# Optimization experiments

Hardware: AMD Instinct MI355X
Metric: run time of the kernel (lower is better)

Reference implementation:

```python
import jax, jax.numpy as jnp
import numpy as np

N = 100000      # nodes
F_IN = 512      # num_features
H = 256         # hidden
C = 64          # num_classes
E = 3200000     # edges
K = 10          # APPNP propagation steps
ALPHA = 0.1     # teleport probability


def setup_inputs() -> dict:
    key = jax.random.key(0)
    k_x, k_w0, k_w1, k_e = jax.random.split(key, 4)
    x = jax.random.normal(k_x, (N, F_IN), dtype=jnp.float32)
    w0 = jax.random.normal(k_w0, (F_IN, H), dtype=jnp.float32) / np.sqrt(F_IN).astype(np.float32)
    b0 = jnp.zeros((H,), dtype=jnp.float32)
    w1 = jax.random.normal(k_w1, (H, C), dtype=jnp.float32) / np.sqrt(H).astype(np.float32)
    b1 = jnpps = jnp.zeros((C,), dtype=jnp.float32)
    edge_index = jax.random.randint(k_e, (2, E), 0, N, dtype=jnp.int64)
    return {"x": x, "w0": w0, "b0": b0, "w1": w1, "b1": b1, "edge_index": edge_index}


def _appnp(h, edge_index):
    # Add self loops (PyG APPNP default: gcn_norm with self loops).
    loops = jnp.arange(N, dtype=edge_index.dtype)
    src = jnp.concatenate([edge_index[0], loops])
    dst = jnp.concatenate([edge_index[1], loops])
    # Symmetric GCN normalization: D^{-1/2} (A+I) D^{-1/2}
    deg = jax.ops.segment_sum(jnp.ones_like(src, dtype=h.dtype), dst, num_segments=N)
    dinv = jnp.where(deg > 0, jax.lax.rsqrt(deg), 0.0)
    norm = dinv[src] * dinv[dst]  # [E+N]

    def step(xc, _):
        msg = norm[:, None] * xc[src]                      # gather [E+N, C]
        agg = jax.ops.segment_sum(msg, dst, num_segments=N)  # scatter-add [N, C]
        return (1.0 - ALPHA) * agg + ALPHA * h, None

    out, _ = jax.lax.scan(step, h, None, length=K)
    return out


def reference(x, w0, b0, w1, b1, edge_index):
    # eval mode: dropout is identity
    h = jax.nn.relu(x @ w0 + b0)   # [N, H]
    h = h @ w1 + b1                # [N, C]
    z = _appnp(h, edge_index)      # [N, C]
    return jax.nn.log_softmax(z, axis=1)
```

## Files before the change

kernel.cpp:

```cpp
#include <hip/hip_runtime.h>
#include <hip/hip_bf16.h>

#define NN 100000
#define EE 3200000
#define FIN 512
#define HH 256
#define CC 64
#define KSTEPS 10
#define SB 391
#define NBUC 782
#define EPB 4096
#define NEB 782
#define NB_X2B 2048
#define NB_PREP 576

typedef __attribute__((ext_vector_type(8))) short bf16x8;
typedef __attribute__((ext_vector_type(8))) short s16x8;
typedef __attribute__((ext_vector_type(4))) float f32x4;
typedef unsigned short ushort_t;

__device__ __forceinline__ short f2bf(float f) {
    union { __hip_bfloat16 h; short s; } u;
    u.h = __float2bfloat16(f);
    return u.s;
}

__device__ __forceinline__ void glds16(const void* g, void* l) {
    __builtin_amdgcn_global_load_lds(
        (const __attribute__((address_space(1))) void*)g,
        (__attribute__((address_space(3))) void*)l, 16, 0, 0);
}


__device__ void dev_x2b(int bx, const float* __restrict__ x, ushort_t* __restrict__ xb) {
    const long NTOT = (long)NN * FIN;
    const long stride = (long)NB_X2B * 256 * 8;
    for (long i = ((long)bx * 256 + threadIdx.x) * 8; i < NTOT; i += stride) {
        float4 a = *(const float4*)(x + i);
        float4 b = *(const float4*)(x + i + 4);
        s16x8 o;
        o[0] = f2bf(a.x); o[1] = f2bf(a.y); o[2] = f2bf(a.z); o[3] = f2bf(a.w);
        o[4] = f2bf(b.x); o[5] = f2bf(b.y); o[6] = f2bf(b.z); o[7] = f2bf(b.w);
        *(s16x8*)(xb + i) = o;
    }
}

__device__ void dev_prep_w(int bx, const float* __restrict__ w0, const float* __restrict__ w1,
                           short* __restrict__ w0t, short* __restrict__ w1t) {
    int t = bx * 256 + threadIdx.x;
    if (t < FIN * HH) {
        int k = t >> 8, n = t & 255;
        w0t[n * FIN + k] = f2bf(w0[t]);
    } else if (t < FIN * HH + HH * CC) {
        int u = t - FIN * HH;
        int k = u >> 6, n = u & 63;
        w1t[n * HH + k] = f2bf(w1[u]);
    }
}

__device__ void dev_bincnt(int bx, const int* __restrict__ ei, int* __restrict__ bcnt,
                           int* __restrict__ hb) {
    int tid = threadIdx.x;
    int base = bx * EPB;
    for (int i = tid; i < NBUC; i += 256) hb[i] = 0;
    __syncthreads();
#pragma unroll 4
    for (int i = 0; i < EPB / 256; ++i) {
        int t = base + i * 256 + tid;
        if (t < EE) atomicAdd(&hb[(unsigned)ei[EE + t] >> 7], 1);
    }
    __syncthreads();
    for (int i = tid; i < NBUC; i += 256)
        if (hb[i]) atomicAdd(&bcnt[i], hb[i]);
}

__global__ __launch_bounds__(256) void fused1(const float* __restrict__ x,
                                              ushort_t* __restrict__ xb,
                                              const int* __restrict__ ei,
                                              int* __restrict__ bcnt,
                                              const float* __restrict__ w0,
                                              const float* __restrict__ w1,
                                              short* __restrict__ w0t,
                                              short* __restrict__ w1t) {
    __shared__ int hb[NBUC];
    int bx = blockIdx.x;
    if (bx < NB_X2B) dev_x2b(bx, x, xb);
    else if (bx < NB_X2B + NEB) dev_bincnt(bx - NB_X2B, ei, bcnt, hb);
    else dev_prep_w(bx - NB_X2B - NEB, w0, w1, w0t, w1t);
}


__global__ __launch_bounds__(1024) void bscan(const int* __restrict__ bcnt,
                                              int* __restrict__ eboff) {
    __shared__ int sh[1024];
    int t = threadIdx.x;
    int v = (t < NBUC) ? bcnt[t] : 0;
    sh[t] = v;
    __syncthreads();
    for (int off = 1; off < 1024; off <<= 1) {
        int add = (t >= off) ? sh[t - off] : 0;
        __syncthreads();
        sh[t] += add;
        __syncthreads();
    }
    if (t < NBUC) eboff[t] = sh[t] - v;
}

__device__ void dev_binfill(int bx, const int* __restrict__ ei, const int* __restrict__ eboff,
                            int* __restrict__ bfc, int* __restrict__ stg, int* pool) {
    int* hb = pool;
    int* lb = pool + NBUC;
    int tid = threadIdx.x;
    int base = bx * EPB;
    for (int i = tid; i < NBUC; i += 256) hb[i] = 0;
    __syncthreads();
#pragma unroll 4
    for (int i = 0; i < EPB / 256; ++i) {
        int t = base + i * 256 + tid;
        if (t < EE) atomicAdd(&hb[(unsigned)ei[EE + t] >> 7], 1);
    }
    __syncthreads();
    for (int i = tid; i < NBUC; i += 256) {
        int c = hb[i];
        lb[i] = eboff[i] + (c ? atomicAdd(&bfc[i], c) : 0);
        hb[i] = 0;
    }
    __syncthreads();
#pragma unroll 4
    for (int i = 0; i < EPB / 256; ++i) {
        int t = base + i * 256 + tid;
        if (t < EE) {
            int s = ei[t];
            int d = ei[EE + t];
            int b = (unsigned)d >> 7;
            int o = atomicAdd(&hb[b], 1);
            stg[lb[b] + o] = (s << 7) | (d & 127);
        }
    }
}

__device__ void dev_gemm1(int g1, const ushort_t* __restrict__ xb,
                          const short* __restrict__ w0t, const float* __restrict__ b0,
                          short* __restrict__ h0, char* sm) {
    short* AsP = (short*)sm;
    short* BsP = (short*)(sm + 32768);
    const int tid = threadIdx.x;
    const int lane = tid & 63;
    const int wid = tid >> 6;
    const int wm = wid >> 1, wn = wid & 1;
    const int bn0 = (g1 & 1) * 128;
    const long row0 = (long)(g1 >> 1) * 128;
    const int rl = lane >> 3;
    const int gko = (lane & 7) ^ rl;

    auto stage = [&](int kt, int buf) {
#pragma unroll
        for (int j = 0; j < 4; ++j) {
            int blk = wid * 4 + j;
            const ushort_t* g = xb + (row0 + blk * 8 + rl) * FIN + kt * 64 + gko * 8;
            glds16(g, &AsP[buf * 8192 + blk * 512]);
        }
#pragma unroll
        for (int j = 0; j < 4; ++j) {
            int blk = wid * 4 + j;
            const short* g = w0t + (size_t)(bn0 + blk * 8 + rl) * FIN + kt * 64 + gko * 8;
            glds16(g, &BsP[buf * 8192 + blk * 512]);
        }
    };

    f32x4 acc[4][4] = {};
    stage(0, 0);
    __syncthreads();
    for (int kt = 0; kt < FIN / 64; ++kt) {
        int cur = kt & 1;
        if (kt < FIN / 64 - 1) stage(kt + 1, cur ^ 1);
#pragma unroll
        for (int ks = 0; ks < 2; ++ks) {
            int ko = ks * 4 + (lane >> 4);
            int slot = ko ^ (lane & 7);
            bf16x8 af[4], bfr[4];
#pragma unroll
            for (int i = 0; i < 4; ++i) {
                int row = wm * 64 + i * 16 + (lane & 15);
                af[i] = *(const bf16x8*)(&AsP[cur * 8192 + (row * 8 + slot) * 8]);
            }
#pragma unroll
            for (int j = 0; j < 4; ++j) {
                int col = wn * 64 + j * 16 + (lane & 15);
                bfr[j] = *(const bf16x8*)(&BsP[cur * 8192 + (col * 8 + slot) * 8]);
            }
#pragma unroll
            for (int i = 0; i < 4; ++i)
#pragma unroll
                for (int j = 0; j < 4; ++j)
                    acc[i][j] = __builtin_amdgcn_mfma_f32_16x16x32_bf16(af[i], bfr[j], acc[i][j], 0, 0, 0);
        }
        __syncthreads();
    }
#pragma unroll
    for (int j = 0; j < 4; ++j) {
        int gcol = bn0 + wn * 64 + j * 16 + (lane & 15);
        float bias = b0[gcol];
#pragma unroll
        for (int i = 0; i < 4; ++i)
#pragma unroll
            for (int q = 0; q < 4; ++q) {
                long grow = row0 + wm * 64 + i * 16 + (lane >> 4) * 4 + q;
                float v = acc[i][j][q] + bias;
                if (v < 0.f) v = 0.f;
                h0[grow * HH + gcol] = f2bf(v);
            }
    }
}

__global__ __launch_bounds__(256) void fused3(const int* __restrict__ ei,
                                              const int* __restrict__ eboff,
                                              int* __restrict__ bfc,
                                              int* __restrict__ stg,
                                              const ushort_t* __restrict__ xb,
                                              const short* __restrict__ w0t,
                                              const float* __restrict__ b0,
                                              short* __restrict__ h0) {
    __shared__ __align__(16) char sm[65536];
    int bx = blockIdx.x, r = bx % 3, q = bx / 3;
    if (r == 2) dev_binfill(q, ei, eboff, bfc, stg, (int*)sm);
    else dev_gemm1(q * 2 + r, xb, w0t, b0, h0, sm);
}

__global__ __launch_bounds__(256) void bucket_finish(
    const int* __restrict__ stg, const int* __restrict__ eboff,
    const int* __restrict__ bcnt,
    int* __restrict__ cnt, float* __restrict__ dinv, float* __restrict__ wco,
    float* __restrict__ sdg, int* __restrict__ rp, int* __restrict__ eds,
    int* __restrict__ dbc) {
    __shared__ int nc8[128 * 8];
    __shared__ int nc[128];
    __shared__ int sc[128];
    __shared__ int lrp[128];
    __shared__ int h64[64];
    int b = blockIdx.x, tid = threadIdx.x;
    int nodes = min(128, NN - b * 128);
    for (int i = tid; i < 128 * 8; i += 256) nc8[i] = 0;
    if (tid < 64) h64[tid] = 0;
    __syncthreads();
    int s0 = eboff[b], n = bcnt[b];
    for (int i = tid; i < n; i += 256) {
        int e = stg[s0 + i];
        atomicAdd(&nc8[(e & 127) * 8 + ((e >> 7) >> 14)], 1);
    }
    __syncthreads();
    if (tid < 128) {
        int excl = 0;
#pragma unroll
        for (int r = 0; r < 8; ++r) {
            int c = nc8[tid * 8 + r];
            nc8[tid * 8 + r] = excl;
            excl += c;
        }
        nc[tid] = excl;
        sc[tid] = (tid < nodes) ? excl + 1 : 0;
    }
    __syncthreads();
    for (int off = 1; off < 128; off <<= 1) {
        int add = (tid < 128 && tid >= off) ? sc[tid - off] : 0;
        __syncthreads();
        if (tid < 128) sc[tid] += add;
        __syncthreads();
    }
    int base = eboff[b] + b * 128;
    if (tid < nodes) {
        int node = b * 128 + tid;
        int c = nc[tid];
        int excl = base + sc[tid] - (c + 1);
        lrp[tid] = excl;
        rp[node] = excl;
        cnt[node] = c;
        float fd = (float)(c + 1);
        dinv[node] = rsqrtf(fd);
        wco[node] = 0.9f / fd;
        sdg[node] = sqrtf(fd);
        atomicAdd(&h64[min(c, 63)], 1);
    }
    if (b == NBUC - 1 && tid == 0) rp[NN] = base + n + nodes;
    __syncthreads();
    if (tid < 64 && h64[tid]) atomicAdd(&dbc[tid], h64[tid]);
    for (int i = tid; i < n; i += 256) {
        int e = stg[s0 + i];
        int src = e >> 7, loc = e & 127;
        int o = atomicAdd(&nc8[loc * 8 + (src >> 14)], 1);
        eds[lrp[loc] + o] = src;
    }
    __syncthreads();
    if (tid < nodes) eds[lrp[tid] + nc[tid]] = b * 128 + tid;
}

__global__ void dscan(const int* __restrict__ dbc, int* __restrict__ dboff) {
    __shared__ int sh[64];
    int t = threadIdx.x;
    int v = dbc[t];
    sh[t] = v;
    __syncthreads();
    for (int off = 1; off < 64; off <<= 1) {
        int add = (t >= off) ? sh[t - off] : 0;
        __syncthreads();
        sh[t] += add;
        __syncthreads();
    }
    dboff[t] = sh[t] - v;
}

__global__ __launch_bounds__(256) void dperm(const int* __restrict__ cnt,
                                             const int* __restrict__ dboff,
                                             int* __restrict__ dfc,
                                             int* __restrict__ perm) {
    __shared__ int h[64];
    __shared__ int base[64];
    int tid = threadIdx.x;
    int i = blockIdx.x * 256 + tid;
    if (tid < 64) h[tid] = 0;
    __syncthreads();
    int bin = 0, r = 0;
    bool ok = i < NN;
    if (ok) {
        bin = min(cnt[i], 63);
        r = atomicAdd(&h[bin], 1);
    }
    __syncthreads();
    if (tid < 64) {
        int c = h[tid];
        base[tid] = dboff[tid] + (c ? atomicAdd(&dfc[tid], c) : 0);
    }
    __syncthreads();
    if (ok) perm[base[bin] + r] = i;
}

__global__ __launch_bounds__(256) void gemm2(const short* __restrict__ h0,
                                             const short* __restrict__ w1t,
                                             const float* __restrict__ b1,
                                             const float* __restrict__ dinv,
                                             ushort_t* __restrict__ hvb,
                                             ushort_t* __restrict__ v0) {
    __shared__ __align__(16) short As[2][128 * 64];
    __shared__ __align__(16) short Bs[2][64 * 64];
    const int tid = threadIdx.x;
    const int lane = tid & 63;
    const int wid = tid >> 6;
    const int wm = wid >> 1, wn = wid & 1;
    const long row0 = (long)blockIdx.x * 128;
    const int rl = lane >> 3;
    const int gko = (lane & 7) ^ rl;

    auto stage = [&](int kt, int buf) {
#pragma unroll
        for (int j = 0; j < 4; ++j) {
            int blk = wid * 4 + j;
            const short* g = h0 + (row0 + blk * 8 + rl) * HH + kt * 64 + gko * 8;
            glds16(g, &As[buf][blk * 512]);
        }
#pragma unroll
        for (int j = 0; j < 2; ++j) {
            int blk = wid * 2 + j;
            const short* g = w1t + (size_t)(blk * 8 + rl) * HH + kt * 64 + gko * 8;
            glds16(g, &Bs[buf][blk * 512]);
        }
    };

    f32x4 acc[4][2] = {};
    stage(0, 0);
    __syncthreads();
    for (int kt = 0; kt < HH / 64; ++kt) {
        int cur = kt & 1;
        if (kt < HH / 64 - 1) stage(kt + 1, cur ^ 1);
#pragma unroll
        for (int ks = 0; ks < 2; ++ks) {
            int ko = ks * 4 + (lane >> 4);
            int slot = ko ^ (lane & 7);
            bf16x8 af[4], bfr[2];
#pragma unroll
            for (int i = 0; i < 4; ++i) {
                int row = wm * 64 + i * 16 + (lane & 15);
                af[i] = *(const bf16x8*)(&As[cur][(row * 8 + slot) * 8]);
            }
#pragma unroll
            for (int j = 0; j < 2; ++j) {
                int col = wn * 32 + j * 16 + (lane & 15);
                bfr[j] = *(const bf16x8*)(&Bs[cur][(col * 8 + slot) * 8]);
            }
#pragma unroll
            for (int i = 0; i < 4; ++i)
#pragma unroll
                for (int j = 0; j < 2; ++j)
                    acc[i][j] = __builtin_amdgcn_mfma_f32_16x16x32_bf16(af[i], bfr[j], acc[i][j], 0, 0, 0);
        }
        __syncthreads();
    }
#pragma unroll
    for (int i = 0; i < 4; ++i)
#pragma unroll
        for (int j = 0; j < 2; ++j) {
            int col = wn * 32 + j * 16 + (lane & 15);
            float bias = b1[col];
#pragma unroll
            for (int q = 0; q < 4; ++q) {
                long grow = row0 + wm * 64 + i * 16 + (lane >> 4) * 4 + q;
                if (grow < NN) {
                    float hval = acc[i][j][q] + bias;
                    float dv = dinv[grow];
                    hvb[grow * CC + col] = (ushort_t)f2bf(0.1f * dv * hval);
                    v0[grow * CC + col] = (ushort_t)f2bf(dv * hval);
                }
            }
        }
}

__device__ __forceinline__ int2 grow2(const ushort_t* __restrict__ vin, int src, int l) {
    return *(const int2*)(vin + ((size_t)src << 6) + (l << 2));
}
__device__ __forceinline__ void acc2(float a[4], int2 r) {
    a[0] += __int_as_float(r.x << 16);
    a[1] += __int_as_float(r.x & 0xffff0000);
    a[2] += __int_as_float(r.y << 16);
    a[3] += __int_as_float(r.y & 0xffff0000);
}

template <int LAST>
__global__ __launch_bounds__(256) void prop(const ushort_t* __restrict__ vin,
                                            const ushort_t* __restrict__ hvb,
                                            const float* __restrict__ wco,
                                            const float* __restrict__ sdg,
                                            ushort_t* __restrict__ vout,
                                            float* __restrict__ zout,
                                            const int* __restrict__ rp,
                                            const int* __restrict__ eds,
                                            const int* __restrict__ perm) {
    int g = perm[blockIdx.x * 16 + (threadIdx.x >> 4)];
    int l = threadIdx.x & 15;
    int beg = rp[g], end = rp[g + 1];
    float a0[4] = {}, a1[4] = {}, a2[4] = {}, a3[4] = {};
    int e = beg;
    int head = (beg + 3) & ~3;
    if (head > end) head = end;
    for (; e < head; ++e) acc2(a0, grow2(vin, eds[e], l));
    for (; e + 7 < end; e += 8) {
        int4 ea = *(const int4*)(eds + e);
        int4 eb = *(const int4*)(eds + e + 4);
        int2 r0 = grow2(vin, ea.x, l);
        int2 r1 = grow2(vin, ea.y, l);
        int2 r2 = grow2(vin, ea.z, l);
        int2 r3 = grow2(vin, ea.w, l);
        int2 r4 = grow2(vin, eb.x, l);
        int2 r5 = grow2(vin, eb.y, l);
        int2 r6 = grow2(vin, eb.z, l);
        int2 r7 = grow2(vin, eb.w, l);
        acc2(a0, r0); acc2(a1, r1); acc2(a2, r2); acc2(a3, r3);
        acc2(a0, r4); acc2(a1, r5); acc2(a2, r6); acc2(a3, r7);
    }
    for (; e + 3 < end; e += 4) {
        int4 ea = *(const int4*)(eds + e);
        int2 r0 = grow2(vin, ea.x, l);
        int2 r1 = grow2(vin, ea.y, l);
        int2 r2 = grow2(vin, ea.z, l);
        int2 r3 = grow2(vin, ea.w, l);
        acc2(a0, r0); acc2(a1, r1); acc2(a2, r2); acc2(a3, r3);
    }
    for (; e < end; ++e) acc2(a1, grow2(vin, eds[e], l));

    float w = wco[g];
    const int2 hb = *(const int2*)(hvb + ((size_t)g << 6) + (l << 2));
    float tv[4];
    tv[0] = __int_as_float(hb.x << 16);
    tv[1] = __int_as_float(hb.x & 0xffff0000);
    tv[2] = __int_as_float(hb.y << 16);
    tv[3] = __int_as_float(hb.y & 0xffff0000);
    float r[4];
#pragma unroll
    for (int c = 0; c < 4; ++c)
        r[c] = w * ((a0[c] + a1[c]) + (a2[c] + a3[c])) + tv[c];
    if (!LAST) {
        int o0 = ((int)(unsigned short)f2bf(r[0])) | (((int)(unsigned short)f2bf(r[1])) << 16);
        int o1 = ((int)(unsigned short)f2bf(r[2])) | (((int)(unsigned short)f2bf(r[3])) << 16);
        *(int2*)(vout + ((size_t)g << 6) + (l << 2)) = make_int2(o0, o1);
    } else {
        float sd = sdg[g];
#pragma unroll
        for (int c = 0; c < 4; ++c) r[c] *= sd;
        float m = fmaxf(fmaxf(r[0], r[1]), fmaxf(r[2], r[3]));
#pragma unroll
        for (int off = 1; off < 16; off <<= 1) m = fmaxf(m, __shfl_xor(m, off));
        float s = expf(r[0] - m) + expf(r[1] - m) + expf(r[2] - m) + expf(r[3] - m);
#pragma unroll
        for (int off = 1; off < 16; off <<= 1) s += __shfl_xor(s, off);
        float ls = m + logf(s);
        f32x4 o;
#pragma unroll
        for (int c = 0; c < 4; ++c) o[c] = r[c] - ls;
        *(f32x4*)(zout + ((size_t)g << 6) + (l << 2)) = o;
    }
}

extern "C" void kernel_launch(void* const* d_in, const int* in_sizes, int n_in,
                              void* d_out, int out_size, void* d_ws, size_t ws_size,
                              hipStream_t stream) {
    const float* x  = (const float*)d_in[0];
    const float* w0 = (const float*)d_in[1];
    const float* b0 = (const float*)d_in[2];
    const float* w1 = (const float*)d_in[3];
    const float* b1 = (const float*)d_in[4];
    const int*   ei = (const int*)d_in[5];

    char* ws = (char*)d_ws;
    size_t off = 0;
    auto take = [&](size_t n) { size_t r = off; off += (n + 255) & ~(size_t)255; return r; };
    size_t o_h0    = take((size_t)100096 * HH * 2);
    size_t o_vA    = take((size_t)NN * CC * 2);
    size_t o_hv    = take((size_t)NN * CC * 2);
    size_t o_ed    = take((size_t)(EE + NN) * 4);
    size_t o_rp    = take((size_t)(NN + 1) * 4);
    size_t o_cnt   = take((size_t)NN * 4);
    size_t o_dinv  = take((size_t)NN * 4);
    size_t o_wco   = take((size_t)NN * 4);
    size_t o_sdg   = take((size_t)NN * 4);
    size_t o_perm  = take((size_t)NN * 4);
    size_t o_w0t   = take((size_t)HH * FIN * 2);
    size_t o_w1t   = take((size_t)CC * HH * 2);
    size_t o_eboff = take((size_t)NBUC * 4);
    size_t o_dboff = take((size_t)64 * 4);
    size_t o_z     = take((size_t)(NBUC + NBUC + 64 + 64) * 4);
    size_t o_xb    = take((size_t)100096 * FIN * 2);

    short*    h0    = (short*)(ws + o_h0);
    ushort_t* vA    = (ushort_t*)(ws + o_vA);
    ushort_t* vB    = (ushort_t*)(ws + o_h0);
    ushort_t* hvb   = (ushort_t*)(ws + o_hv);
    int*      stg   = (int*)(ws + o_hv);
    int*      eds   = (int*)(ws + o_ed);
    int*      rp    = (int*)(ws + o_rp);
    int*      cnt   = (int*)(ws + o_cnt);
    float*    dinv  = (float*)(ws + o_dinv);
    float*    wco   = (float*)(ws + o_wco);
    float*    sdg   = (float*)(ws + o_sdg);
    int*      perm  = (int*)(ws + o_perm);
    short*    w0t   = (short*)(ws + o_w0t);
    short*    w1t   = (short*)(ws + o_w1t);
    int*      eboff = (int*)(ws + o_eboff);
    int*      dboff = (int*)(ws + o_dboff);
    int*      bcnt  = (int*)(ws + o_z);
    int*      bfc   = bcnt + NBUC;
    int*      dbc   = bfc + NBUC;
    int*      dfc   = dbc + 64;
    ushort_t* xb    = (ushort_t*)(ws + o_xb);
    float*    zout  = (float*)d_out;

    hipMemsetAsync(ws + o_z, 0, (size_t)(NBUC + NBUC + 64 + 64) * 4, stream);

    fused1<<<NB_X2B + NEB + NB_PREP, 256, 0, stream>>>(x, xb, ei, bcnt, w0, w1, w0t, w1t);
    bscan<<<1, 1024, 0, stream>>>(bcnt, eboff);
    fused3<<<NBUC * 3, 256, 0, stream>>>(ei, eboff, bfc, stg, xb, w0t, b0, h0);
    bucket_finish<<<NBUC, 256, 0, stream>>>(stg, eboff, bcnt, cnt, dinv, wco, sdg, rp, eds, dbc);
    dscan<<<1, 64, 0, stream>>>(dbc, dboff);
    dperm<<<SB, 256, 0, stream>>>(cnt, dboff, dfc, perm);

    gemm2<<<782, 256, 0, stream>>>(h0, w1t, b1, dinv, hvb, vA);

    const ushort_t* in = vA;
    for (int k = 0; k < KSTEPS; ++k) {
        if (k == KSTEPS - 1) {
            prop<1><<<NN / 16, 256, 0, stream>>>(in, hvb, wco, sdg, nullptr, zout, rp, eds, perm);
        } else {
            ushort_t* o = (k & 1) ? vA : vB;
            prop<0><<<NN / 16, 256, 0, stream>>>(in, hvb, wco, sdg, o, nullptr, rp, eds, perm);
            in = o;
        }
    }
}
```

Baseline: 816.1 us.

## Fuse degree scan, permutation and gemm2 into one launch; refine CSR source sort

Folds the single-block degree-histogram scan into each permutation block, then merges the permutation and the second GEMM into one heterogeneous kernel. This removes two kernel launches and their serialization gaps. Separately, bucket_finish now sorts each node's edge list into 16 source ranges instead of 8, aiming for better gather locality in the propagation steps at the cost of more shared-memory counters and a longer per-node scan. The redundant 64-entry scan in every permutation block adds a little work per block.

```diff
diff --git a/kernel.cpp b/kernel.cpp
--- a/kernel.cpp
+++ b/kernel.cpp
@@ -13,6 +13,7 @@
 #define NEB 782
 #define NB_X2B 2048
 #define NB_PREP 576
+#define NRNG 16
 
 typedef __attribute__((ext_vector_type(8))) short bf16x8;
 typedef __attribute__((ext_vector_type(8))) short s16x8;
@@ -233,28 +234,28 @@
     int* __restrict__ cnt, float* __restrict__ dinv, float* __restrict__ wco,
     float* __restrict__ sdg, int* __restrict__ rp, int* __restrict__ eds,
     int* __restrict__ dbc) {
-    __shared__ int nc8[128 * 8];
+    __shared__ int ncr[128 * NRNG];
     __shared__ int nc[128];
     __shared__ int sc[128];
     __shared__ int lrp[128];
     __shared__ int h64[64];
     int b = blockIdx.x, tid = threadIdx.x;
     int nodes = min(128, NN - b * 128);
-    for (int i = tid; i < 128 * 8; i += 256) nc8[i] = 0;
+    for (int i = tid; i < 128 * NRNG; i += 256) ncr[i] = 0;
     if (tid < 64) h64[tid] = 0;
     __syncthreads();
     int s0 = eboff[b], n = bcnt[b];
     for (int i = tid; i < n; i += 256) {
         int e = stg[s0 + i];
-        atomicAdd(&nc8[(e & 127) * 8 + ((e >> 7) >> 14)], 1);
+        atomicAdd(&ncr[(e & 127) * NRNG + ((e >> 7) >> 13)], 1);
     }
     __syncthreads();
     if (tid < 128) {
         int excl = 0;
 #pragma unroll
-        for (int r = 0; r < 8; ++r) {
-            int c = nc8[tid * 8 + r];
-            nc8[tid * 8 + r] = excl;
+        for (int r = 0; r < NRNG; ++r) {
+            int c = ncr[tid * NRNG + r];
+            ncr[tid * NRNG + r] = excl;
             excl += c;
         }
         nc[tid] = excl;
@@ -287,66 +288,25 @@
     for (int i = tid; i < n; i += 256) {
         int e = stg[s0 + i];
         int src = e >> 7, loc = e & 127;
-        int o = atomicAdd(&nc8[loc * 8 + (src >> 14)], 1);
+        int o = atomicAdd(&ncr[loc * NRNG + (src >> 13)], 1);
         eds[lrp[loc] + o] = src;
     }
     __syncthreads();
     if (tid < nodes) eds[lrp[tid] + nc[tid]] = b * 128 + tid;
 }
 
-__global__ void dscan(const int* __restrict__ dbc, int* __restrict__ dboff) {
-    __shared__ int sh[64];
-    int t = threadIdx.x;
-    int v = dbc[t];
-    sh[t] = v;
-    __syncthreads();
-    for (int off = 1; off < 64; off <<= 1) {
-        int add = (t >= off) ? sh[t - off] : 0;
-        __syncthreads();
-        sh[t] += add;
-        __syncthreads();
-    }
-    dboff[t] = sh[t] - v;
-}
-
-__global__ __launch_bounds__(256) void dperm(const int* __restrict__ cnt,
-                                             const int* __restrict__ dboff,
-                                             int* __restrict__ dfc,
-                                             int* __restrict__ perm) {
-    __shared__ int h[64];
-    __shared__ int base[64];
-    int tid = threadIdx.x;
-    int i = blockIdx.x * 256 + tid;
-    if (tid < 64) h[tid] = 0;
-    __syncthreads();
-    int bin = 0, r = 0;
-    bool ok = i < NN;
-    if (ok) {
-        bin = min(cnt[i], 63);
-        r = atomicAdd(&h[bin], 1);
-    }
-    __syncthreads();
-    if (tid < 64) {
-        int c = h[tid];
-        base[tid] = dboff[tid] + (c ? atomicAdd(&dfc[tid], c) : 0);
-    }
-    __syncthreads();
-    if (ok) perm[base[bin] + r] = i;
-}
-
-__global__ __launch_bounds__(256) void gemm2(const short* __restrict__ h0,
-                                             const short* __restrict__ w1t,
-                                             const float* __restrict__ b1,
-                                             const float* __restrict__ dinv,
-                                             ushort_t* __restrict__ hvb,
-                                             ushort_t* __restrict__ v0) {
-    __shared__ __align__(16) short As[2][128 * 64];
-    __shared__ __align__(16) short Bs[2][64 * 64];
+
+__device__ void dev_gemm2(int g2, const short* __restrict__ h0,
+                          const short* __restrict__ w1t, const float* __restrict__ b1,
+                          const float* __restrict__ dinv,
+                          ushort_t* __restrict__ hvb, ushort_t* __restrict__ v0, char* sm) {
+    short* AsP = (short*)sm;
+    short* BsP = (short*)(sm + 32768);
     const int tid = threadIdx.x;
     const int lane = tid & 63;
     const int wid = tid >> 6;
     const int wm = wid >> 1, wn = wid & 1;
-    const long row0 = (long)blockIdx.x * 128;
+    const long row0 = (long)g2 * 128;
     const int rl = lane >> 3;
     const int gko = (lane & 7) ^ rl;
 
@@ -355,13 +315,13 @@
         for (int j = 0; j < 4; ++j) {
             int blk = wid * 4 + j;
             const short* g = h0 + (row0 + blk * 8 + rl) * HH + kt * 64 + gko * 8;
-            glds16(g, &As[buf][blk * 512]);
+            glds16(g, &AsP[buf * 8192 + blk * 512]);
         }
 #pragma unroll
         for (int j = 0; j < 2; ++j) {
             int blk = wid * 2 + j;
             const short* g = w1t + (size_t)(blk * 8 + rl) * HH + kt * 64 + gko * 8;
-            glds16(g, &Bs[buf][blk * 512]);
+            glds16(g, &BsP[buf * 4096 + blk * 512]);
         }
     };
 
@@ -379,12 +339,12 @@
 #pragma unroll
             for (int i = 0; i < 4; ++i) {
                 int row = wm * 64 + i * 16 + (lane & 15);
-                af[i] = *(const bf16x8*)(&As[cur][(row * 8 + slot) * 8]);
+                af[i] = *(const bf16x8*)(&AsP[cur * 8192 + (row * 8 + slot) * 8]);
             }
 #pragma unroll
             for (int j = 0; j < 2; ++j) {
                 int col = wn * 32 + j * 16 + (lane & 15);
-                bfr[j] = *(const bf16x8*)(&Bs[cur][(col * 8 + slot) * 8]);
+                bfr[j] = *(const bf16x8*)(&BsP[cur * 4096 + (col * 8 + slot) * 8]);
             }
 #pragma unroll
             for (int i = 0; i < 4; ++i)
@@ -411,6 +371,52 @@
                 }
             }
         }
+}
+
+__device__ void dev_dperm(int bx, const int* __restrict__ cnt, const int* __restrict__ dbc,
+                          int* __restrict__ dfc, int* __restrict__ perm, int* pool) {
+    int* h    = pool;
+    int* base = pool + 64;
+    int* sh   = pool + 128;
+    int tid = threadIdx.x;
+    if (tid < 64) { h[tid] = 0; sh[tid] = dbc[tid]; }
+    __syncthreads();
+    for (int off = 1; off < 64; off <<= 1) {
+        int add = (tid < 64 && tid >= off) ? sh[tid - off] : 0;
+        __syncthreads();
+        if (tid < 64) sh[tid] += add;
+        __syncthreads();
+    }
+    int i = bx * 256 + tid;
+    int bin = 0, r = 0;
+    bool ok = i < NN;
+    if (ok) {
+        bin = min(cnt[i], 63);
+        r = atomicAdd(&h[bin], 1);
+    }
+    __syncthreads();
+    if (tid < 64) {
+        int c = h[tid];
+        base[tid] = (sh[tid] - dbc[tid]) + (c ? atomicAdd(&dfc[tid], c) : 0);
+    }
+    __syncthreads();
+    if (ok) perm[base[bin] + r] = i;
+}
+
+__global__ __launch_bounds__(256) void fused5(const short* __restrict__ h0,
+                                              const short* __restrict__ w1t,
+                                              const float* __restrict__ b1,
+                                              const float* __restrict__ dinv,
+                                              ushort_t* __restrict__ hvb,
+                                              ushort_t* __restrict__ v0,
+                                              const int* __restrict__ cnt,
+                                              const int* __restrict__ dbc,
+                                              int* __restrict__ dfc,
+                                              int* __restrict__ perm) {
+    __shared__ __align__(16) char sm[49152];
+    int bx = blockIdx.x;
+    if (bx < NBUC) dev_gemm2(bx, h0, w1t, b1, dinv, hvb, v0, sm);
+    else dev_dperm(bx - NBUC, cnt, dbc, dfc, perm, (int*)sm);
 }
 
 __device__ __forceinline__ int2 grow2(const ushort_t* __restrict__ vin, int src, int l) {
@@ -524,7 +530,6 @@
     size_t o_w0t   = take((size_t)HH * FIN * 2);
     size_t o_w1t   = take((size_t)CC * HH * 2);
     size_t o_eboff = take((size_t)NBUC * 4);
-    size_t o_dboff = take((size_t)64 * 4);
     size_t o_z     = take((size_t)(NBUC + NBUC + 64 + 64) * 4);
     size_t o_xb    = take((size_t)100096 * FIN * 2);
 
@@ -543,7 +548,6 @@
     short*    w0t   = (short*)(ws + o_w0t);
     short*    w1t   = (short*)(ws + o_w1t);
     int*      eboff = (int*)(ws + o_eboff);
-    int*      dboff = (int*)(ws + o_dboff);
     int*      bcnt  = (int*)(ws + o_z);
     int*      bfc   = bcnt + NBUC;
     int*      dbc   = bfc + NBUC;
@@ -557,10 +561,7 @@
     bscan<<<1, 1024, 0, stream>>>(bcnt, eboff);
     fused3<<<NBUC * 3, 256, 0, stream>>>(ei, eboff, bfc, stg, xb, w0t, b0, h0);
     bucket_finish<<<NBUC, 256, 0, stream>>>(stg, eboff, bcnt, cnt, dinv, wco, sdg, rp, eds, dbc);
-    dscan<<<1, 64, 0, stream>>>(dbc, dboff);
-    dperm<<<SB, 256, 0, stream>>>(cnt, dboff, dfc, perm);
-
-    gemm2<<<782, 256, 0, stream>>>(h0, w1t, b1, dinv, hvb, vA);
+    fused5<<<NBUC + SB, 256, 0, stream>>>(h0, w1t, b1, dinv, hvb, vA, cnt, dbc, dfc, perm);
 
     const ushort_t* in = vA;
     for (int k = 0; k < KSTEPS; ++k) {
```

After: 807.4 us. Within noise of the previous version (-1.1%).
